# Optimization experiments

Hardware: AMD Instinct MI355X
Metric: run time of the kernel (lower is better)

Reference implementation:

```python
import jax, jax.numpy as jnp
import numpy as np

B, S, D, H, F = 4, 2048, 1024, 16, 4096
HD = D // H
NEG = -2.0 ** 32
EPS = 1e-5


def _gelu(x):
    return x * 0.5 * (1.0 + jax.scipy.special.erf(x / jnp.sqrt(2.0).astype(x.dtype)))


def _layernorm(x, scale, offset):
    mu = jnp.mean(x, axis=-1, keepdims=True)
    var = jnp.mean(jnp.square(x - mu), axis=-1, keepdims=True)
    return (x - mu) * jax.lax.rsqrt(var + EPS) * scale + offset


def setup_inputs() -> dict:
    key = jax.random.key(0)
    ks = jax.random.split(key, 12)
    s = 0.02
    return {
        "x": jax.random.normal(ks[0], (B, S, D), jnp.float32),
        "mask": jnp.zeros((B, S), jnp.int32),  # 1 = masked-out (padding)
        "Wq": jax.random.normal(ks[1], (D, D), jnp.float32) * s,
        "bq": jnp.zeros((D,), jnp.float32),
        "Wk": jax.random.normal(ks[2], (D, D), jnp.float32) * s,
        "bk": jnp.zeros((D,), jnp.float32),
        "Wv": jax.random.normal(ks[3], (D, D), jnp.float32) * s,
        "bv": jnp.zeros((D,), jnp.float32),
        "Wo": jax.random.normal(ks[4], (D, D), jnp.float32) * s,
        "bo": jnp.zeros((D,), jnp.float32),
        "ln1_s": jnp.ones((D,), jnp.float32),
        "ln1_b": jnp.zeros((D,), jnp.float32),
        "W1": jax.random.normal(ks[5], (D, F), jnp.float32) * s,
        "b1": jnp.zeros((F,), jnp.float32),
        "W2": jax.random.normal(ks[6], (F, D), jnp.float32) * s,
        "b2": jnp.zeros((D,), jnp.float32),
        "ln2_s": jnp.ones((D,), jnp.float32),
        "ln2_b": jnp.zeros((D,), jnp.float32),
    }


def reference(x, mask, Wq, bq, Wk, bk, Wv, bv, Wo, bo, ln1_s, ln1_b,
              W1, b1, W2, b2, ln2_s, ln2_b):
    b, s, d = x.shape
    q = (x @ Wq + bq).reshape(b, s, H, HD)
    k = (x @ Wk + bk).reshape(b, s, H, HD)
    v = (x @ Wv + bv).reshape(b, s, H, HD)
    logits = jnp.einsum('btnh,bsnh->bnts', q, k) / jnp.sqrt(jnp.float32(HD))
    logits = logits + (mask.astype(jnp.float32) * NEG)[:, None, None, :]
    attn = jax.nn.softmax(logits, axis=-1)
    ctx = jnp.einsum('bsnh,bnts->btnh', v, attn).reshape(b, s, d)
    attn_out = ctx @ Wo + bo
    h = _layernorm(attn_out + x, ln1_s, ln1_b)
    mlp = _gelu(h @ W1 + b1) @ W2 + b2
    return _layernorm(mlp + h, ln2_s, ln2_b)
```

## Files before the change

kernel.cpp:

```cpp
#include <hip/hip_runtime.h>
#include <hip/hip_bf16.h>

typedef __attribute__((ext_vector_type(8))) short short8;
typedef __attribute__((ext_vector_type(4))) short s16x4;
typedef __attribute__((ext_vector_type(4))) float f32x4;
typedef unsigned short u16;

#define DEV __device__ __forceinline__
#define MFMA32(a, b, c) __builtin_amdgcn_mfma_f32_16x16x32_bf16(a, b, c, 0, 0, 0)
#define MFMA16(a, b, c) __builtin_amdgcn_mfma_f32_16x16x16bf16_1k(a, b, c, 0, 0, 0)

DEV u16 f2b(float f) {
    __hip_bfloat16 h = __float2bfloat16(f);
    return __builtin_bit_cast(unsigned short, h);
}

DEV float max3f(float a, float b, float c) {
    float d;
    asm("v_max3_f32 %0, %1, %2, %3" : "=v"(d) : "v"(a), "v"(b), "v"(c));
    return d;
}

DEV void gl_lds16(const u16* g, u16* l) {
    __builtin_amdgcn_global_load_lds((const unsigned int*)g, (unsigned int*)l, 16, 0, 0);
}

__global__ __launch_bounds__(256) void cast_bf16(const float* __restrict__ in, u16* __restrict__ out, int n) {
    int i = (blockIdx.x * 256 + threadIdx.x) * 4;
    if (i < n) {
        float4 v = *(const float4*)(in + i);
        ushort4 o;
        o.x = f2b(v.x); o.y = f2b(v.y); o.z = f2b(v.z); o.w = f2b(v.w);
        *(ushort4*)(out + i) = o;
    }
}

__global__ __launch_bounds__(256) void transpose_cast(const float* __restrict__ in, u16* __restrict__ out,
                                                      int R, int C) {
    __shared__ float t[32][33];
    int bx = blockIdx.x * 32;
    int by = blockIdx.y * 32;
    int tx = threadIdx.x, ty = threadIdx.y;
#pragma unroll
    for (int i = 0; i < 32; i += 8) t[ty + i][tx] = in[(size_t)(by + ty + i) * C + bx + tx];
    __syncthreads();
#pragma unroll
    for (int i = 0; i < 32; i += 8) out[(size_t)(bx + ty + i) * R + by + tx] = f2b(t[tx][ty + i]);
}

__global__ __launch_bounds__(256) void pack_bias(const float* __restrict__ bq, const float* __restrict__ bk,
                                                 const float* __restrict__ bv, const float* __restrict__ bo,
                                                 const float* __restrict__ b1, const float* __restrict__ b2,
                                                 float* __restrict__ out) {
    int i = blockIdx.x * 256 + threadIdx.x;
    if (i >= 9216) return;
    float v;
    if (i < 1024) v = bq[i];
    else if (i < 2048) v = bk[i - 1024];
    else if (i < 3072) v = bv[i - 2048];
    else if (i < 4096) v = bo[i - 3072];
    else if (i < 8192) v = b1[i - 4096];
    else v = b2[i - 8192];
    out[i] = v;
}

template <bool GELU, bool BF16OUT, bool RESID>
__global__ __launch_bounds__(256) void gemm_bt(const u16* __restrict__ A, const u16* __restrict__ B,
                                               const float* __restrict__ bias, float* __restrict__ cf,
                                               u16* __restrict__ cb, const float* __restrict__ res,
                                               int M, int N, int K) {
    __shared__ __align__(16) u16 As[128 * 64];
    __shared__ __align__(16) u16 Bs[128 * 64];
    const int tid = threadIdx.x;
    const int wid = tid >> 6, lane = tid & 63;
    const int wr = wid >> 1, wc = wid & 1;
    const int m0 = blockIdx.x * 128, n0 = blockIdx.y * 128;
    const int r16 = lane & 15, g = lane >> 4;
    const int sw = r16 & 7;

    f32x4 acc[4][4];
#pragma unroll
    for (int i = 0; i < 4; i++)
#pragma unroll
        for (int j = 0; j < 4; j++) acc[i][j] = (f32x4){0.f, 0.f, 0.f, 0.f};

    const int srow = tid >> 3;
    const int schunk = (tid & 7) ^ (srow & 7);
    const u16* ga = A + (size_t)(m0 + srow) * K + schunk * 8;
    const u16* gb = B + (size_t)(n0 + srow) * K + schunk * 8;

    for (int kt = 0; kt < K; kt += 64) {
#pragma unroll
        for (int j = 0; j < 4; j++) {
            gl_lds16(ga + (size_t)(j * 32) * K + kt, &As[(j * 32 + wid * 8) * 64]);
            gl_lds16(gb + (size_t)(j * 32) * K + kt, &Bs[(j * 32 + wid * 8) * 64]);
        }
        __syncthreads();
#pragma unroll
        for (int ks = 0; ks < 2; ks++) {
            short8 af[4], bfr[4];
#pragma unroll
            for (int i = 0; i < 4; i++) {
                int row = wr * 64 + i * 16 + r16;
                af[i] = *(const short8*)((const char*)As + row * 128 + (((ks * 4 + g) ^ sw) * 16));
            }
#pragma unroll
            for (int j = 0; j < 4; j++) {
                int row = wc * 64 + j * 16 + r16;
                bfr[j] = *(const short8*)((const char*)Bs + row * 128 + (((ks * 4 + g) ^ sw) * 16));
            }
#pragma unroll
            for (int i = 0; i < 4; i++)
#pragma unroll
                for (int j = 0; j < 4; j++) acc[i][j] = MFMA32(af[i], bfr[j], acc[i][j]);
        }
        __syncthreads();
    }

#pragma unroll
    for (int i = 0; i < 4; i++) {
#pragma unroll
        for (int j = 0; j < 4; j++) {
#pragma unroll
            for (int r = 0; r < 4; r++) {
                int row = m0 + wr * 64 + i * 16 + g * 4 + r;
                int col = n0 + wc * 64 + j * 16 + r16;
                float v = acc[i][j][r] + bias[col];
                if (RESID) v += res[(size_t)row * N + col];
                if (GELU) v = 0.5f * v * (1.0f + erff(v * 0.70710678118654752f));
                if (BF16OUT) cb[(size_t)row * N + col] = f2b(v);
                else cf[(size_t)row * N + col] = v;
            }
        }
    }
}

__global__ __launch_bounds__(256, 4) void attn_kernel(const u16* __restrict__ qkv, const int* __restrict__ mask,
                                                      u16* __restrict__ ctx) {
    const int tid = threadIdx.x, wid = tid >> 6, lane = tid & 63;
    const int r16 = lane & 15, g = lane >> 4;
    const int h = blockIdx.y, b = blockIdx.z;
    const size_t baserow = (size_t)b * 2048;
    const int q0 = blockIdx.x * 128;

    __shared__ __align__(16) u16 Ks[64 * 64];
    __shared__ __align__(16) u16 Vs[64 * 64];
    __shared__ unsigned tflags_sh;

    const float SCALE = 0.18033688011112042f;
    const float MNEG = -6.196328018e9f;
    const s16x4 ONES = {(short)0x3F80, (short)0x3F80, (short)0x3F80, (short)0x3F80};

    short8 qfA0, qfA1, qfB0, qfB1;
    {
        const u16* qp = qkv + (baserow + q0 + wid * 32 + r16) * 3072 + h * 64 + g * 8;
        qfA0 = *(const short8*)qp;
        qfA1 = *(const short8*)(qp + 32);
        qfB0 = *(const short8*)(qp + (size_t)16 * 3072);
        qfB1 = *(const short8*)(qp + (size_t)16 * 3072 + 32);
    }

    if (tid == 0) tflags_sh = 0;
    __syncthreads();
    for (int r = 0; r < 8; ++r) {
        int v = mask[baserow + r * 256 + tid];
        unsigned long long bal = __ballot(v != 0);
        if (bal != 0 && lane == 0) atomicOr(&tflags_sh, 1u << (r * 4 + wid));
    }

    const int L = lane;
    const u16* kg0 = qkv + (baserow + wid * 16 + (L >> 3)) * 3072 + 1024 + h * 64 + ((L & 7) ^ (L >> 3)) * 8;
    const u16* kg1 = kg0 + (size_t)8 * 3072;
    u16* kl0 = &Ks[wid * 1024];
    u16* kl1 = &Ks[wid * 1024 + 512];
    const u16* vg0 = qkv + (baserow + wid * 16 + ((L & 31) >> 1)) * 3072 + 2048 + h * 64
                     + ((L >> 5) * 16 + (L & 1) * 8);
    const u16* vg1 = vg0 + 32;
    u16* vl0 = &Vs[wid * 1024];
    u16* vl1 = &Vs[wid * 1024 + 512];
    const unsigned vaddr = (unsigned)(unsigned long long)&Vs[0] + (unsigned)(r16 * 2 + g * 128);

    __syncthreads();
    const unsigned tfl = tflags_sh;

    f32x4 OtA[4], OtB[4];
#pragma unroll
    for (int dt = 0; dt < 4; dt++) { OtA[dt] = (f32x4){0.f, 0.f, 0.f, 0.f}; OtB[dt] = (f32x4){0.f, 0.f, 0.f, 0.f}; }
    f32x4 OsumA = (f32x4){0.f, 0.f, 0.f, 0.f}, OsumB = (f32x4){0.f, 0.f, 0.f, 0.f};
    float mrunA = -1e30f, mrunB = -1e30f;

    for (int t = 0; t < 32; ++t) {
        const int kt = t * 64;
        const size_t go = (size_t)kt * 3072;
        gl_lds16(kg0 + go, kl0);
        gl_lds16(kg1 + go, kl1);
        gl_lds16(vg0 + go, vl0);
        gl_lds16(vg1 + go, vl1);
        __syncthreads();

        f32x4 zA[4], zB[4];
        __builtin_amdgcn_s_setprio(1);
#pragma unroll
        for (int tt = 0; tt < 4; tt++) {
            const int row = tt * 16 + r16;
            const int swz = row & 7;
            short8 a0 = *(const short8*)&Ks[row * 64 + ((g ^ swz) * 8)];
            short8 a1 = *(const short8*)&Ks[row * 64 + (((4 + g) ^ swz) * 8)];
            f32x4 za = (f32x4){0.f, 0.f, 0.f, 0.f};
            za = MFMA32(a0, qfA0, za);
            za = MFMA32(a1, qfA1, za);
            zA[tt] = za;
            f32x4 zb = (f32x4){0.f, 0.f, 0.f, 0.f};
            zb = MFMA32(a0, qfB0, zb);
            zb = MFMA32(a1, qfB1, zb);
            zB[tt] = zb;
        }
        __builtin_amdgcn_s_setprio(0);

        float a0_ = max3f(zA[0][0], zA[0][1], zA[0][2]);
        float a1_ = max3f(zA[0][3], zA[1][0], zA[1][1]);
        float a2_ = max3f(zA[1][2], zA[1][3], zA[2][0]);
        float a3_ = max3f(zA[2][1], zA[2][2], zA[2][3]);
        float a4_ = max3f(zA[3][0], zA[3][1], zA[3][2]);
        float zmaxA = fmaxf(max3f(a0_, a1_, a2_), max3f(a3_, a4_, zA[3][3]));
        float b0_ = max3f(zB[0][0], zB[0][1], zB[0][2]);
        float b1_ = max3f(zB[0][3], zB[1][0], zB[1][1]);
        float b2_ = max3f(zB[1][2], zB[1][3], zB[2][0]);
        float b3_ = max3f(zB[2][1], zB[2][2], zB[2][3]);
        float b4_ = max3f(zB[3][0], zB[3][1], zB[3][2]);
        float zmaxB = fmaxf(max3f(b0_, b1_, b2_), max3f(b3_, b4_, zB[3][3]));
        zmaxA = fmaxf(zmaxA, __shfl_xor(zmaxA, 16));
        zmaxB = fmaxf(zmaxB, __shfl_xor(zmaxB, 16));
        zmaxA = fmaxf(zmaxA, __shfl_xor(zmaxA, 32));
        zmaxB = fmaxf(zmaxB, __shfl_xor(zmaxB, 32));
        float pmaxA = zmaxA * SCALE, pmaxB = zmaxB * SCALE;

        if (!__all(pmaxA - mrunA <= 11.5f)) {
            float mnew = fmaxf(mrunA, pmaxA);
            float alpha = exp2f(mrunA - mnew);
            mrunA = mnew;
            OsumA *= alpha;
#pragma unroll
            for (int dt = 0; dt < 4; dt++) OtA[dt] *= alpha;
        }
        if (!__all(pmaxB - mrunB <= 11.5f)) {
            float mnew = fmaxf(mrunB, pmaxB);
            float alpha = exp2f(mrunB - mnew);
            mrunB = mnew;
            OsumB *= alpha;
#pragma unroll
            for (int dt = 0; dt < 4; dt++) OtB[dt] *= alpha;
        }

        s16x4 pbA[4], pbB[4];
        const float negmA = -mrunA, negmB = -mrunB;
        if (__builtin_expect((tfl >> t) & 1u, 0)) {
            const int* mrow = mask + baserow + kt;
#pragma unroll
            for (int tt = 0; tt < 4; tt++) {
                float pa[4], pbv[4];
#pragma unroll
                for (int j = 0; j < 4; j++) {
                    float mbj = mrow[tt * 16 + g * 4 + j] ? MNEG : 0.0f;
                    pa[j] = exp2f(__builtin_fmaf(zA[tt][j], SCALE, mbj + negmA));
                    pbv[j] = exp2f(__builtin_fmaf(zB[tt][j], SCALE, mbj + negmB));
                }
                unsigned lo, hi;
                asm("v_cvt_pk_bf16_f32 %0, %1, %2" : "=v"(lo) : "v"(pa[0]), "v"(pa[1]));
                asm("v_cvt_pk_bf16_f32 %0, %1, %2" : "=v"(hi) : "v"(pa[2]), "v"(pa[3]));
                uint2 ua; ua.x = lo; ua.y = hi;
                pbA[tt] = __builtin_bit_cast(s16x4, ua);
                asm("v_cvt_pk_bf16_f32 %0, %1, %2" : "=v"(lo) : "v"(pbv[0]), "v"(pbv[1]));
                asm("v_cvt_pk_bf16_f32 %0, %1, %2" : "=v"(hi) : "v"(pbv[2]), "v"(pbv[3]));
                uint2 ub; ub.x = lo; ub.y = hi;
                pbB[tt] = __builtin_bit_cast(s16x4, ub);
            }
        } else {
#pragma unroll
            for (int tt = 0; tt < 4; tt++) {
                float pa0 = exp2f(__builtin_fmaf(zA[tt][0], SCALE, negmA));
                float pa1 = exp2f(__builtin_fmaf(zA[tt][1], SCALE, negmA));
                float pa2 = exp2f(__builtin_fmaf(zA[tt][2], SCALE, negmA));
                float pa3 = exp2f(__builtin_fmaf(zA[tt][3], SCALE, negmA));
                float pb0 = exp2f(__builtin_fmaf(zB[tt][0], SCALE, negmB));
                float pb1 = exp2f(__builtin_fmaf(zB[tt][1], SCALE, negmB));
                float pb2 = exp2f(__builtin_fmaf(zB[tt][2], SCALE, negmB));
                float pb3 = exp2f(__builtin_fmaf(zB[tt][3], SCALE, negmB));
                unsigned lo, hi;
                asm("v_cvt_pk_bf16_f32 %0, %1, %2" : "=v"(lo) : "v"(pa0), "v"(pa1));
                asm("v_cvt_pk_bf16_f32 %0, %1, %2" : "=v"(hi) : "v"(pa2), "v"(pa3));
                uint2 ua; ua.x = lo; ua.y = hi;
                pbA[tt] = __builtin_bit_cast(s16x4, ua);
                asm("v_cvt_pk_bf16_f32 %0, %1, %2" : "=v"(lo) : "v"(pb0), "v"(pb1));
                asm("v_cvt_pk_bf16_f32 %0, %1, %2" : "=v"(hi) : "v"(pb2), "v"(pb3));
                uint2 ub; ub.x = lo; ub.y = hi;
                pbB[tt] = __builtin_bit_cast(s16x4, ub);
            }
        }

        s16x4 vf[2][4];
#pragma unroll
        for (int dt = 0; dt < 4; dt++)
            asm volatile("ds_read_b64_tr_b16 %0, %1"
                         : "=v"(vf[0][dt]) : "v"(vaddr + (unsigned)(dt * 512)));
#pragma unroll
        for (int tt = 0; tt < 4; tt++) {
            if (tt < 3) {
#pragma unroll
                for (int dt = 0; dt < 4; dt++)
                    asm volatile("ds_read_b64_tr_b16 %0, %1"
                                 : "=v"(vf[(tt + 1) & 1][dt])
                                 : "v"(vaddr + (unsigned)(((tt + 1) * 4 + dt) * 512)));
                asm volatile("s_waitcnt lgkmcnt(4)" ::: "memory");
            } else {
                asm volatile("s_waitcnt lgkmcnt(0)" ::: "memory");
            }
            __builtin_amdgcn_sched_barrier(0);
            __builtin_amdgcn_s_setprio(1);
#pragma unroll
            for (int dt = 0; dt < 4; dt++) {
                OtA[dt] = MFMA16(vf[tt & 1][dt], pbA[tt], OtA[dt]);
                OtB[dt] = MFMA16(vf[tt & 1][dt], pbB[tt], OtB[dt]);
            }
            OsumA = MFMA16(ONES, pbA[tt], OsumA);
            OsumB = MFMA16(ONES, pbB[tt], OsumB);
            __builtin_amdgcn_s_setprio(0);
        }
        __syncthreads();
    }

    const float rlA = 1.0f / OsumA[0];
    const float rlB = 1.0f / OsumB[0];
    u16* cpA = ctx + (baserow + q0 + wid * 32 + r16) * 1024 + h * 64 + g * 4;
    u16* cpB = cpA + (size_t)16 * 1024;
#pragma unroll
    for (int dt = 0; dt < 4; dt++) {
        ushort4 oa, ob;
        oa.x = f2b(OtA[dt][0] * rlA); oa.y = f2b(OtA[dt][1] * rlA);
        oa.z = f2b(OtA[dt][2] * rlA); oa.w = f2b(OtA[dt][3] * rlA);
        ob.x = f2b(OtB[dt][0] * rlB); ob.y = f2b(OtB[dt][1] * rlB);
        ob.z = f2b(OtB[dt][2] * rlB); ob.w = f2b(OtB[dt][3] * rlB);
        *(ushort4*)(cpA + dt * 16) = oa;
        *(ushort4*)(cpB + dt * 16) = ob;
    }
}

__global__ __launch_bounds__(256) void ln_kernel(const float* __restrict__ a, const float* __restrict__ res,
                                                 const float* __restrict__ gamma, const float* __restrict__ beta,
                                                 float* __restrict__ outf, u16* __restrict__ outb) {
    const int row = blockIdx.x, tid = threadIdx.x;
    const size_t base = (size_t)row * 1024 + tid * 4;
    float4 va = *(const float4*)(a + base);
    float x0 = va.x, x1 = va.y, x2 = va.z, x3 = va.w;
    if (res) {
        float4 vr = *(const float4*)(res + base);
        x0 += vr.x; x1 += vr.y; x2 += vr.z; x3 += vr.w;
    }
    float s = x0 + x1 + x2 + x3;
    float ss = x0 * x0 + x1 * x1 + x2 * x2 + x3 * x3;
#pragma unroll
    for (int m = 1; m < 64; m <<= 1) { s += __shfl_xor(s, m, 64); ss += __shfl_xor(ss, m, 64); }
    __shared__ float red[8];
    if ((tid & 63) == 0) { red[tid >> 6] = s; red[4 + (tid >> 6)] = ss; }
    __syncthreads();
    s = red[0] + red[1] + red[2] + red[3];
    ss = red[4] + red[5] + red[6] + red[7];
    float mu = s * (1.0f / 1024.0f);
    float var = ss * (1.0f / 1024.0f) - mu * mu;
    float rstd = rsqrtf(var + 1e-5f);
    float4 g4 = *(const float4*)(gamma + tid * 4);
    float4 b4 = *(const float4*)(beta + tid * 4);
    float y0 = (x0 - mu) * rstd * g4.x + b4.x;
    float y1 = (x1 - mu) * rstd * g4.y + b4.y;
    float y2 = (x2 - mu) * rstd * g4.z + b4.z;
    float y3 = (x3 - mu) * rstd * g4.w + b4.w;
    *(float4*)(outf + base) = make_float4(y0, y1, y2, y3);
    if (outb) {
        ushort4 ob;
        ob.x = f2b(y0); ob.y = f2b(y1); ob.z = f2b(y2); ob.w = f2b(y3);
        *(ushort4*)(outb + base) = ob;
    }
}

extern "C" void kernel_launch(void* const* d_in, const int* in_sizes, int n_in, void* d_out, int out_size,
                              void* d_ws, size_t ws_size, hipStream_t stream) {
    const float* x = (const float*)d_in[0];
    const int* mask = (const int*)d_in[1];
    const float* Wq = (const float*)d_in[2];
    const float* bq = (const float*)d_in[3];
    const float* Wk = (const float*)d_in[4];
    const float* bk = (const float*)d_in[5];
    const float* Wv = (const float*)d_in[6];
    const float* bv = (const float*)d_in[7];
    const float* Wo = (const float*)d_in[8];
    const float* bo = (const float*)d_in[9];
    const float* ln1s = (const float*)d_in[10];
    const float* ln1b = (const float*)d_in[11];
    const float* W1 = (const float*)d_in[12];
    const float* b1 = (const float*)d_in[13];
    const float* W2 = (const float*)d_in[14];
    const float* b2 = (const float*)d_in[15];
    const float* ln2s = (const float*)d_in[16];
    const float* ln2b = (const float*)d_in[17];
    float* out = (float*)d_out;
    char* ws = (char*)d_ws;

    const size_t MB = 1024 * 1024;
    u16* XB = (u16*)(ws + 0);
    u16* WTq = (u16*)(ws + 16 * MB);
    u16* WTk = WTq + 1024 * 1024;
    u16* WTv = WTk + 1024 * 1024;
    u16* WTo = WTv + 1024 * 1024;
    u16* WT1 = WTo + 1024 * 1024;
    u16* WT2 = WT1 + 4096 * 1024;
    float* BIAS = (float*)(ws + 40 * MB);
    u16* QKV = (u16*)(ws + 41 * MB);
    u16* CTX = (u16*)(ws + 0);
    float* ATT = (float*)(ws + 41 * MB);
    float* Hbuf = (float*)(ws + 73 * MB);
    u16* HB = (u16*)(ws + 105 * MB);
    u16* MLP1 = (u16*)(ws + 121 * MB);
    float* MLP2 = (float*)(ws + 41 * MB);

    dim3 tb(32, 8);
    cast_bf16<<<8192, 256, 0, stream>>>(x, XB, 8192 * 1024);
    transpose_cast<<<dim3(32, 32), tb, 0, stream>>>(Wq, WTq, 1024, 1024);
    transpose_cast<<<dim3(32, 32), tb, 0, stream>>>(Wk, WTk, 1024, 1024);
    transpose_cast<<<dim3(32, 32), tb, 0, stream>>>(Wv, WTv, 1024, 1024);
    transpose_cast<<<dim3(32, 32), tb, 0, stream>>>(Wo, WTo, 1024, 1024);
    transpose_cast<<<dim3(128, 32), tb, 0, stream>>>(W1, WT1, 1024, 4096);
    transpose_cast<<<dim3(32, 128), tb, 0, stream>>>(W2, WT2, 4096, 1024);
    pack_bias<<<36, 256, 0, stream>>>(bq, bk, bv, bo, b1, b2, BIAS);

    gemm_bt<false, true, false><<<dim3(64, 24), 256, 0, stream>>>(XB, WTq, BIAS, nullptr, QKV, nullptr, 8192, 3072, 1024);
    attn_kernel<<<dim3(16, 16, 4), 256, 0, stream>>>(QKV, mask, CTX);
    gemm_bt<false, false, true><<<dim3(64, 8), 256, 0, stream>>>(CTX, WTo, BIAS + 3072, ATT, nullptr, x, 8192, 1024, 1024);
    ln_kernel<<<8192, 256, 0, stream>>>(ATT, nullptr, ln1s, ln1b, Hbuf, HB);
    gemm_bt<true, true, false><<<dim3(64, 32), 256, 0, stream>>>(HB, WT1, BIAS + 4096, nullptr, MLP1, nullptr, 8192, 4096, 1024);
    gemm_bt<false, false, true><<<dim3(64, 8), 256, 0, stream>>>(MLP1, WT2, BIAS + 8192, MLP2, nullptr, Hbuf, 8192, 1024, 4096);
    ln_kernel<<<8192, 256, 0, stream>>>(MLP2, nullptr, ln2s, ln2b, out, nullptr);
}
```

Measured before the change: 486.1 us.

## Split attention key range across two wave groups with LDS merge

The attention block doubles to 512 threads. Two groups of four waves each process half of the key sequence for the same 128 queries, each with its own K/V LDS buffers and online softmax state. At the end the second half writes its partial outputs, running max and sum to LDS, and the first half combines them flash-decoding style before writing ctx. This halves the serial key loop per wave and adds more waves per CU to hide latency, at the cost of a final merge, more LDS and higher register pressure under the new launch bounds.

Result: slower. 1.398 ms (+187.7%).

```diff
diff --git a/kernel.cpp b/kernel.cpp
--- a/kernel.cpp
+++ b/kernel.cpp
@@ -135,16 +135,17 @@
     }
 }
 
-__global__ __launch_bounds__(256, 4) void attn_kernel(const u16* __restrict__ qkv, const int* __restrict__ mask,
+__global__ __launch_bounds__(512, 8) void attn_kernel(const u16* __restrict__ qkv, const int* __restrict__ mask,
                                                       u16* __restrict__ ctx) {
     const int tid = threadIdx.x, wid = tid >> 6, lane = tid & 63;
+    const int half = wid >> 2, w4 = wid & 3;
     const int r16 = lane & 15, g = lane >> 4;
     const int h = blockIdx.y, b = blockIdx.z;
     const size_t baserow = (size_t)b * 2048;
     const int q0 = blockIdx.x * 128;
 
-    __shared__ __align__(16) u16 Ks[64 * 64];
-    __shared__ __align__(16) u16 Vs[64 * 64];
+    __shared__ __align__(16) u16 KV[2][2][64 * 64];
+    __shared__ float ml[4][2][2][16];
     __shared__ unsigned tflags_sh;
 
     const float SCALE = 0.18033688011112042f;
@@ -153,7 +154,7 @@
 
     short8 qfA0, qfA1, qfB0, qfB1;
     {
-        const u16* qp = qkv + (baserow + q0 + wid * 32 + r16) * 3072 + h * 64 + g * 8;
+        const u16* qp = qkv + (baserow + q0 + w4 * 32 + r16) * 3072 + h * 64 + g * 8;
         qfA0 = *(const short8*)qp;
         qfA1 = *(const short8*)(qp + 32);
         qfB0 = *(const short8*)(qp + (size_t)16 * 3072);
@@ -162,23 +163,25 @@
 
     if (tid == 0) tflags_sh = 0;
     __syncthreads();
-    for (int r = 0; r < 8; ++r) {
-        int v = mask[baserow + r * 256 + tid];
+    for (int r = 0; r < 4; ++r) {
+        int v = mask[baserow + r * 512 + tid];
         unsigned long long bal = __ballot(v != 0);
-        if (bal != 0 && lane == 0) atomicOr(&tflags_sh, 1u << (r * 4 + wid));
+        if (bal != 0 && lane == 0) atomicOr(&tflags_sh, 1u << (r * 8 + wid));
     }
 
     const int L = lane;
-    const u16* kg0 = qkv + (baserow + wid * 16 + (L >> 3)) * 3072 + 1024 + h * 64 + ((L & 7) ^ (L >> 3)) * 8;
+    const size_t keybase = baserow + half * 1024;
+    const u16* kg0 = qkv + (keybase + w4 * 16 + (L >> 3)) * 3072 + 1024 + h * 64 + ((L & 7) ^ (L >> 3)) * 8;
     const u16* kg1 = kg0 + (size_t)8 * 3072;
-    u16* kl0 = &Ks[wid * 1024];
-    u16* kl1 = &Ks[wid * 1024 + 512];
-    const u16* vg0 = qkv + (baserow + wid * 16 + ((L & 31) >> 1)) * 3072 + 2048 + h * 64
+    u16* kl0 = &KV[half][0][w4 * 1024];
+    u16* kl1 = kl0 + 512;
+    const u16* vg0 = qkv + (keybase + w4 * 16 + ((L & 31) >> 1)) * 3072 + 2048 + h * 64
                      + ((L >> 5) * 16 + (L & 1) * 8);
     const u16* vg1 = vg0 + 32;
-    u16* vl0 = &Vs[wid * 1024];
-    u16* vl1 = &Vs[wid * 1024 + 512];
-    const unsigned vaddr = (unsigned)(unsigned long long)&Vs[0] + (unsigned)(r16 * 2 + g * 128);
+    u16* vl0 = &KV[half][1][w4 * 1024];
+    u16* vl1 = vl0 + 512;
+    const u16* Ks = &KV[half][0][0];
+    const unsigned vaddr = (unsigned)(unsigned long long)&KV[half][1][0] + (unsigned)(r16 * 2 + g * 128);
 
     __syncthreads();
     const unsigned tfl = tflags_sh;
@@ -189,9 +192,8 @@
     f32x4 OsumA = (f32x4){0.f, 0.f, 0.f, 0.f}, OsumB = (f32x4){0.f, 0.f, 0.f, 0.f};
     float mrunA = -1e30f, mrunB = -1e30f;
 
-    for (int t = 0; t < 32; ++t) {
-        const int kt = t * 64;
-        const size_t go = (size_t)kt * 3072;
+    for (int t = 0; t < 16; ++t) {
+        const size_t go = (size_t)(t * 64) * 3072;
         gl_lds16(kg0 + go, kl0);
         gl_lds16(kg1 + go, kl1);
         gl_lds16(vg0 + go, vl0);
@@ -254,8 +256,9 @@
 
         s16x4 pbA[4], pbB[4];
         const float negmA = -mrunA, negmB = -mrunB;
-        if (__builtin_expect((tfl >> t) & 1u, 0)) {
-            const int* mrow = mask + baserow + kt;
+        const int gtile = half * 16 + t;
+        if (__builtin_expect((tfl >> gtile) & 1u, 0)) {
+            const int* mrow = mask + keybase + t * 64;
 #pragma unroll
             for (int tt = 0; tt < 4; tt++) {
                 float pa[4], pbv[4];
@@ -329,19 +332,50 @@
         __syncthreads();
     }
 
-    const float rlA = 1.0f / OsumA[0];
-    const float rlB = 1.0f / OsumB[0];
-    u16* cpA = ctx + (baserow + q0 + wid * 32 + r16) * 1024 + h * 64 + g * 4;
-    u16* cpB = cpA + (size_t)16 * 1024;
-#pragma unroll
-    for (int dt = 0; dt < 4; dt++) {
-        ushort4 oa, ob;
-        oa.x = f2b(OtA[dt][0] * rlA); oa.y = f2b(OtA[dt][1] * rlA);
-        oa.z = f2b(OtA[dt][2] * rlA); oa.w = f2b(OtA[dt][3] * rlA);
-        ob.x = f2b(OtB[dt][0] * rlB); ob.y = f2b(OtB[dt][1] * rlB);
-        ob.z = f2b(OtB[dt][2] * rlB); ob.w = f2b(OtB[dt][3] * rlB);
-        *(ushort4*)(cpA + dt * 16) = oa;
-        *(ushort4*)(cpB + dt * 16) = ob;
+    float* fb = (float*)&KV[0][0][0];
+    if (half) {
+        float* dst = fb + w4 * 2048 + lane * 32;
+#pragma unroll
+        for (int dt = 0; dt < 4; dt++) {
+            *(f32x4*)(dst + dt * 4) = OtA[dt];
+            *(f32x4*)(dst + 16 + dt * 4) = OtB[dt];
+        }
+        if (g == 0) {
+            ml[w4][0][0][r16] = mrunA;
+            ml[w4][0][1][r16] = OsumA[0];
+            ml[w4][1][0][r16] = mrunB;
+            ml[w4][1][1][r16] = OsumB[0];
+        }
+    }
+    __syncthreads();
+    if (!half) {
+        float mA2 = ml[w4][0][0][r16], lA2 = ml[w4][0][1][r16];
+        float mB2 = ml[w4][1][0][r16], lB2 = ml[w4][1][1][r16];
+        float nmA = fmaxf(mrunA, mA2);
+        float aA1 = exp2f(mrunA - nmA), aA2 = exp2f(mA2 - nmA);
+        float nmB = fmaxf(mrunB, mB2);
+        float aB1 = exp2f(mrunB - nmB), aB2 = exp2f(mB2 - nmB);
+        const float rlA = 1.0f / (OsumA[0] * aA1 + lA2 * aA2);
+        const float rlB = 1.0f / (OsumB[0] * aB1 + lB2 * aB2);
+        const float* src = fb + w4 * 2048 + lane * 32;
+        u16* cpA = ctx + (baserow + q0 + w4 * 32 + r16) * 1024 + h * 64 + g * 4;
+        u16* cpB = cpA + (size_t)16 * 1024;
+#pragma unroll
+        for (int dt = 0; dt < 4; dt++) {
+            f32x4 pA = *(const f32x4*)(src + dt * 4);
+            f32x4 pB = *(const f32x4*)(src + 16 + dt * 4);
+            ushort4 oa, ob;
+            oa.x = f2b((OtA[dt][0] * aA1 + pA[0] * aA2) * rlA);
+            oa.y = f2b((OtA[dt][1] * aA1 + pA[1] * aA2) * rlA);
+            oa.z = f2b((OtA[dt][2] * aA1 + pA[2] * aA2) * rlA);
+            oa.w = f2b((OtA[dt][3] * aA1 + pA[3] * aA2) * rlA);
+            ob.x = f2b((OtB[dt][0] * aB1 + pB[0] * aB2) * rlB);
+            ob.y = f2b((OtB[dt][1] * aB1 + pB[1] * aB2) * rlB);
+            ob.z = f2b((OtB[dt][2] * aB1 + pB[2] * aB2) * rlB);
+            ob.w = f2b((OtB[dt][3] * aB1 + pB[3] * aB2) * rlB);
+            *(ushort4*)(cpA + dt * 16) = oa;
+            *(ushort4*)(cpB + dt * 16) = ob;
+        }
     }
 }
 
@@ -433,7 +467,7 @@
     pack_bias<<<36, 256, 0, stream>>>(bq, bk, bv, bo, b1, b2, BIAS);
 
     gemm_bt<false, true, false><<<dim3(64, 24), 256, 0, stream>>>(XB, WTq, BIAS, nullptr, QKV, nullptr, 8192, 3072, 1024);
-    attn_kernel<<<dim3(16, 16, 4), 256, 0, stream>>>(QKV, mask, CTX);
+    attn_kernel<<<dim3(16, 16, 4), 512, 0, stream>>>(QKV, mask, CTX);
     gemm_bt<false, false, true><<<dim3(64, 8), 256, 0, stream>>>(CTX, WTo, BIAS + 3072, ATT, nullptr, x, 8192, 1024, 1024);
     ln_kernel<<<8192, 256, 0, stream>>>(ATT, nullptr, ln1s, ln1b, Hbuf, HB);
     gemm_bt<true, true, false><<<dim3(64, 32), 256, 0, stream>>>(HB, WT1, BIAS + 4096, nullptr, MLP1, nullptr, 8192, 4096, 1024);
```

## Double-buffer K/V tiles in attention kernel to overlap loads with compute

Applied to the files above, without the earlier changes.

Allocates two LDS buffers for K and V and issues the global-to-LDS loads for the next key tile before computing on the current one. Explicit vmcnt waits and raw s_barrier replace __syncthreads so the prefetch stays in flight during the QK and PV MFMAs. This hides global load latency at the cost of doubled LDS use (32KB per block), which may reduce occupancy, and of relying on hand-placed waitcnt correctness.

New measurement: 473.9 us. 1.03x faster.

```diff
diff --git a/kernel.cpp b/kernel.cpp
--- a/kernel.cpp
+++ b/kernel.cpp
@@ -9,6 +9,7 @@
 #define DEV __device__ __forceinline__
 #define MFMA32(a, b, c) __builtin_amdgcn_mfma_f32_16x16x32_bf16(a, b, c, 0, 0, 0)
 #define MFMA16(a, b, c) __builtin_amdgcn_mfma_f32_16x16x16bf16_1k(a, b, c, 0, 0, 0)
+#define SBAR() asm volatile("s_barrier" ::: "memory")
 
 DEV u16 f2b(float f) {
     __hip_bfloat16 h = __float2bfloat16(f);
@@ -143,8 +144,8 @@
     const size_t baserow = (size_t)b * 2048;
     const int q0 = blockIdx.x * 128;
 
-    __shared__ __align__(16) u16 Ks[64 * 64];
-    __shared__ __align__(16) u16 Vs[64 * 64];
+    __shared__ __align__(16) u16 Ks[2][64 * 64];
+    __shared__ __align__(16) u16 Vs[2][64 * 64];
     __shared__ unsigned tflags_sh;
 
     const float SCALE = 0.18033688011112042f;
@@ -171,15 +172,15 @@
     const int L = lane;
     const u16* kg0 = qkv + (baserow + wid * 16 + (L >> 3)) * 3072 + 1024 + h * 64 + ((L & 7) ^ (L >> 3)) * 8;
     const u16* kg1 = kg0 + (size_t)8 * 3072;
-    u16* kl0 = &Ks[wid * 1024];
-    u16* kl1 = &Ks[wid * 1024 + 512];
     const u16* vg0 = qkv + (baserow + wid * 16 + ((L & 31) >> 1)) * 3072 + 2048 + h * 64
                      + ((L >> 5) * 16 + (L & 1) * 8);
     const u16* vg1 = vg0 + 32;
-    u16* vl0 = &Vs[wid * 1024];
-    u16* vl1 = &Vs[wid * 1024 + 512];
-    const unsigned vaddr = (unsigned)(unsigned long long)&Vs[0] + (unsigned)(r16 * 2 + g * 128);
-
+    const unsigned vaddr0 = (unsigned)(unsigned long long)&Vs[0][0] + (unsigned)(r16 * 2 + g * 128);
+
+    gl_lds16(kg0, &Ks[0][wid * 1024]);
+    gl_lds16(kg1, &Ks[0][wid * 1024 + 512]);
+    gl_lds16(vg0, &Vs[0][wid * 1024]);
+    gl_lds16(vg1, &Vs[0][wid * 1024 + 512]);
     __syncthreads();
     const unsigned tfl = tflags_sh;
 
@@ -190,13 +191,20 @@
     float mrunA = -1e30f, mrunB = -1e30f;
 
     for (int t = 0; t < 32; ++t) {
-        const int kt = t * 64;
-        const size_t go = (size_t)kt * 3072;
-        gl_lds16(kg0 + go, kl0);
-        gl_lds16(kg1 + go, kl1);
-        gl_lds16(vg0 + go, vl0);
-        gl_lds16(vg1 + go, vl1);
-        __syncthreads();
+        const int cur = t & 1, nb = cur ^ 1;
+        if (t < 31) {
+            const size_t go = (size_t)(t + 1) * 64 * 3072;
+            gl_lds16(kg0 + go, &Ks[nb][wid * 1024]);
+            gl_lds16(kg1 + go, &Ks[nb][wid * 1024 + 512]);
+            gl_lds16(vg0 + go, &Vs[nb][wid * 1024]);
+            gl_lds16(vg1 + go, &Vs[nb][wid * 1024 + 512]);
+            asm volatile("s_waitcnt vmcnt(4)" ::: "memory");
+        } else {
+            asm volatile("s_waitcnt vmcnt(0)" ::: "memory");
+        }
+        SBAR();
+        const u16* Kc = &Ks[cur][0];
+        const unsigned vaddr = vaddr0 + (unsigned)(cur * 8192);
 
         f32x4 zA[4], zB[4];
         __builtin_amdgcn_s_setprio(1);
@@ -204,8 +212,8 @@
         for (int tt = 0; tt < 4; tt++) {
             const int row = tt * 16 + r16;
             const int swz = row & 7;
-            short8 a0 = *(const short8*)&Ks[row * 64 + ((g ^ swz) * 8)];
-            short8 a1 = *(const short8*)&Ks[row * 64 + (((4 + g) ^ swz) * 8)];
+            short8 a0 = *(const short8*)&Kc[row * 64 + ((g ^ swz) * 8)];
+            short8 a1 = *(const short8*)&Kc[row * 64 + (((4 + g) ^ swz) * 8)];
             f32x4 za = (f32x4){0.f, 0.f, 0.f, 0.f};
             za = MFMA32(a0, qfA0, za);
             za = MFMA32(a1, qfA1, za);
@@ -255,7 +263,7 @@
         s16x4 pbA[4], pbB[4];
         const float negmA = -mrunA, negmB = -mrunB;
         if (__builtin_expect((tfl >> t) & 1u, 0)) {
-            const int* mrow = mask + baserow + kt;
+            const int* mrow = mask + baserow + t * 64;
 #pragma unroll
             for (int tt = 0; tt < 4; tt++) {
                 float pa[4], pbv[4];
@@ -326,7 +334,7 @@
             OsumB = MFMA16(ONES, pbB[tt], OsumB);
             __builtin_amdgcn_s_setprio(0);
         }
-        __syncthreads();
+        SBAR();
     }
 
     const float rlA = 1.0f / OsumA[0];
```
